# Kernel optimization log

Measured on AMD Instinct MI355X. Metric: run time of the kernel, lower is better.

The kernel has to match this reference:

```python
import jax, jax.numpy as jnp
import numpy as np

NUM_HEADS = 16
NEG_INF = -9e15


def setup_inputs() -> dict:
    key = jax.random.key(0)
    k1, k2, k3 = jax.random.split(key, 3)
    B, S, D = 2, 2048, 1024
    # xavier-uniform-ish init scale for weights
    lim_qkv = float(np.sqrt(6.0 / (D + 3 * D)))
    lim_o = float(np.sqrt(6.0 / (D + D)))
    return {
        "x": jax.random.normal(k1, (B, S, D), dtype=jnp.float32),
        "w_qkv": jax.random.uniform(k2, (3 * D, D), minval=-lim_qkv, maxval=lim_qkv, dtype=jnp.float32),
        "b_qkv": jnp.zeros((3 * D,), dtype=jnp.float32),
        "w_o": jax.random.uniform(k3, (D, D), minval=-lim_o, maxval=lim_o, dtype=jnp.float32),
        "b_o": jnp.zeros((D,), dtype=jnp.float32),
    }


def reference(x, w_qkv, b_qkv, w_o, b_o):
    B, S, D = x.shape
    H = NUM_HEADS
    hd = D // H
    # qkv projection: [B,S,3D]
    qkv = x @ w_qkv.T + b_qkv
    # -> [B, H, S, 3*hd], then split
    qkv = qkv.reshape(B, S, H, 3 * hd).transpose(0, 2, 1, 3)
    q, k, v = jnp.split(qkv, 3, axis=-1)  # each [B,H,S,hd]
    scale = 1.0 / jnp.sqrt(jnp.asarray(hd, dtype=x.dtype))
    logits = jnp.einsum("bhqd,bhkd->bhqk", q, k) * scale
    attn = jax.nn.softmax(logits, axis=-1)
    vals = jnp.einsum("bhqk,bhkd->bhqd", attn, v)
    vals = vals.transpose(0, 2, 1, 3).reshape(B, S, D)
    return vals @ w_o.T + b_o
```

## Files before the change

### kernel.cpp

```cpp
#include <hip/hip_runtime.h>
#include <math.h>

#define NHEADS 16
#define HD 64

typedef __attribute__((ext_vector_type(8))) _Float16 half8;
typedef __attribute__((ext_vector_type(4))) _Float16 half4;
typedef __attribute__((ext_vector_type(4))) float f32x4;
typedef __attribute__((ext_vector_type(16))) float f32x16;
typedef __attribute__((ext_vector_type(4))) unsigned int u32x4;

__device__ inline void load_lds16(const void* g, void* l) {
    __builtin_amdgcn_global_load_lds(
        (const __attribute__((address_space(1))) unsigned int*)g,
        (__attribute__((address_space(3))) unsigned int*)l, 16, 0, 0);
}
__device__ inline void pl32swap(unsigned int& x, unsigned int& y) {
    asm volatile("v_permlane32_swap_b32 %0, %1" : "+v"(x), "+v"(y));
}

#define NX  4194304
#define NWQ 3145728
#define NWO 1048576
__global__ void cvt_all(const float* __restrict__ x, const float* __restrict__ wq,
                        const float* __restrict__ wo, _Float16* __restrict__ xf,
                        _Float16* __restrict__ wqf, _Float16* __restrict__ wof) {
    int i = (blockIdx.x * blockDim.x + threadIdx.x) * 8;
    const float* src; _Float16* dst; int off;
    if (i < NX)            { src = x;  dst = xf;  off = i; }
    else if (i < NX + NWQ) { src = wq; dst = wqf; off = i - NX; }
    else                   { src = wo; dst = wof; off = i - (NX + NWQ); }
    float4 a = *(const float4*)(src + off);
    float4 b = *(const float4*)(src + off + 4);
    half8 h;
    h[0] = (_Float16)a.x; h[1] = (_Float16)a.y; h[2] = (_Float16)a.z; h[3] = (_Float16)a.w;
    h[4] = (_Float16)b.x; h[5] = (_Float16)b.y; h[6] = (_Float16)b.z; h[7] = (_Float16)b.w;
    *(half8*)(dst + off) = h;
}

#define GEMM_CORE(K)                                                                   \
    __shared__ __align__(1024) unsigned char smem[16384];                              \
    const int tid = threadIdx.x;                                                       \
    const int l = tid & 63, w = tid >> 6;                                              \
    const int wr = w >> 1, wc = w & 1;                                                 \
    const int nwg = gridDim.x * gridDim.y;                                             \
    const int bid = blockIdx.y * gridDim.x + blockIdx.x;                               \
    const int swz = (bid & 7) * (nwg >> 3) + (bid >> 3);                               \
    const int m0 = (swz / gridDim.x) * 128, n0 = (swz % gridDim.x) * 128;              \
    const int srow = tid >> 2;                                                         \
    const int schunk = (tid & 3) ^ ((srow >> 1) & 3);                                  \
    const size_t gA0 = (size_t)(m0 + srow) * K + schunk * 8;                           \
    const size_t gA1 = gA0 + (size_t)64 * K;                                           \
    const size_t gB0 = (size_t)(n0 + srow) * K + schunk * 8;                           \
    const size_t gB1 = gB0 + (size_t)64 * K;                                           \
    unsigned char* ldsW = smem + w * 1024;                                             \
    const int col16 = l & 15, kc = l >> 4;                                             \
    const int ra0 = wr * 64 + col16;                                                   \
    const int offA = ra0 * 64 + ((kc ^ ((ra0 >> 1) & 3)) * 16);                        \
    const int rb0 = wc * 64 + col16;                                                   \
    const int offB = rb0 * 64 + ((kc ^ ((rb0 >> 1) & 3)) * 16);                        \
    f32x4 acc[4][4] = {};                                                              \
    for (int k0 = 0; k0 < K; k0 += 32) {                                               \
        load_lds16(A + gA0 + k0, ldsW + 0);                                            \
        load_lds16(A + gA1 + k0, ldsW + 4096);                                         \
        load_lds16(B + gB0 + k0, ldsW + 8192);                                         \
        load_lds16(B + gB1 + k0, ldsW + 12288);                                       \
        __syncthreads();                                                               \
        half8 af[4], bf[4];                                                            \
        _Pragma("unroll")                                                              \
        for (int m = 0; m < 4; ++m) af[m] = *(const half8*)(smem + offA + m * 1024);   \
        _Pragma("unroll")                                                              \
        for (int n = 0; n < 4; ++n) bf[n] = *(const half8*)(smem + 8192 + offB + n * 1024); \
        _Pragma("unroll")                                                              \
        for (int m = 0; m < 4; ++m)                                                    \
            _Pragma("unroll")                                                          \
            for (int n = 0; n < 4; ++n)                                                \
                acc[m][n] = __builtin_amdgcn_mfma_f32_16x16x32_f16(af[m], bf[n], acc[m][n], 0, 0, 0); \
        __syncthreads();                                                               \
    }

__global__ __launch_bounds__(256, 2) void gemm_o(
    const _Float16* __restrict__ A, const _Float16* __restrict__ B,
    const float* __restrict__ bias, float* __restrict__ C,
    int M, int N, int K) {
    GEMM_CORE(K)
    const int rowb = m0 + wr * 64 + (l >> 4) * 4;
    const int colb = n0 + wc * 64 + col16;
    float bv[4];
    #pragma unroll
    for (int n = 0; n < 4; ++n) bv[n] = bias[colb + n * 16];
    #pragma unroll
    for (int m = 0; m < 4; ++m)
        #pragma unroll
        for (int j = 0; j < 4; ++j) {
            float* crow = C + (size_t)(rowb + m * 16 + j) * N + colb;
            #pragma unroll
            for (int n = 0; n < 4; ++n) crow[n * 16] = acc[m][n][j] + bv[n];
        }
}

#define QSCALE 0.18033688f
__global__ __launch_bounds__(256, 2) void gemm_qkv(
    const _Float16* __restrict__ A, const _Float16* __restrict__ B,
    const float* __restrict__ bias,
    _Float16* __restrict__ Qf, _Float16* __restrict__ Kf,
    _Float16* __restrict__ VfT, int K) {
    GEMM_CORE(K)
    const int rowb = m0 + wr * 64 + (l >> 4) * 4;
    const int colb = n0 + wc * 64 + col16;
    #pragma unroll
    for (int n = 0; n < 4; ++n) {
        int col = colb + n * 16;
        int h = col / 192;
        int rem = col - h * 192;
        int part = rem >> 6, d = rem & 63;
        float bv = bias[col];
        #pragma unroll
        for (int m = 0; m < 4; ++m) {
            int r0 = rowb + m * 16;
            int b = r0 >> 11, s0r = r0 & 2047;
            int bh = b * 16 + h;
            if (part == 0) {
                #pragma unroll
                for (int j = 0; j < 4; ++j)
                    Qf[((size_t)bh * 2048 + s0r + j) * 64 + d] =
                        (_Float16)((acc[m][n][j] + bv) * QSCALE);
            } else if (part == 1) {
                #pragma unroll
                for (int j = 0; j < 4; ++j)
                    Kf[((size_t)bh * 2048 + s0r + j) * 64 + d] = (_Float16)(acc[m][n][j] + bv);
            } else {
                half4 pk;
                pk[0] = (_Float16)(acc[m][n][0] + bv);
                pk[1] = (_Float16)(acc[m][n][1] + bv);
                pk[2] = (_Float16)(acc[m][n][2] + bv);
                pk[3] = (_Float16)(acc[m][n][3] + bv);
                *(half4*)&VfT[((size_t)bh * 64 + d) * 2048 + s0r] = pk;
            }
        }
    }
}

__global__ __launch_bounds__(256, 2) void mfma_attn(
    const _Float16* __restrict__ Qf, const _Float16* __restrict__ Kf,
    const _Float16* __restrict__ VfT, _Float16* __restrict__ vals) {
    __shared__ __align__(1024) unsigned char smem[32768];
    const int tid = threadIdx.x;
    const int l = tid & 63, w = tid >> 6;
    const int l31 = l & 31, hl = l >> 5;
    const int bh = blockIdx.y, q0 = blockIdx.x * 128;
    const int h = bh & 15, b = bh >> 4;

    half8 qf[4];
    {
        const _Float16* qp = Qf + ((size_t)bh * 2048 + q0 + w * 32 + l31) * 64 + hl * 8;
        #pragma unroll
        for (int c = 0; c < 4; ++c) qf[c] = *(const half8*)(qp + c * 16);
    }
    f32x16 zvec = {};
    f32x16 o0 = {}, o1 = {};
    float mshift = 0.f, lsum = 0.f;

    const _Float16* Kg = Kf + (size_t)bh * 2048 * 64;
    const _Float16* Vg = VfT + (size_t)bh * 64 * 2048;

    int offK[2], offV[2];
    #pragma unroll
    for (int i = 0; i < 2; ++i) {
        int row2 = w * 8 + i * 4 + (l >> 4);
        int slot = (l & 15) ^ (row2 & 15);
        int row = row2 * 2 + (slot >> 3);
        int chunk = slot & 7;
        offK[i] = row * 64 + chunk * 8;
        offV[i] = row * 2048 + chunk * 8;
    }
    const int sbase = (l31 & 1) * 8;
    const int xr = (l31 >> 1) & 15;
    const int rb0 = (l31 >> 1) * 256;

    #define STAGE(kt0, buf)                                                            \
        {                                                                              \
            unsigned char* bK = smem + (buf) * 8192 + w * 2048;                        \
            unsigned char* bV = smem + 16384 + (buf) * 8192 + w * 2048;                \
            load_lds16(Kg + (size_t)(kt0) * 64 + offK[0], bK);                         \
            load_lds16(Kg + (size_t)(kt0) * 64 + offK[1], bK + 1024);                  \
            load_lds16(Vg + (kt0) + offV[0], bV);                                      \
            load_lds16(Vg + (kt0) + offV[1], bV + 1024);                               \
        }

    STAGE(0, 0)
    __syncthreads();
    int cur = 0;
    for (int t = 0; t < 32; ++t) {
        if (t + 1 < 32) STAGE((t + 1) * 64, cur ^ 1)
        const unsigned char* Ksb = smem + cur * 8192;
        const unsigned char* Vsb = smem + 16384 + cur * 8192;

        f32x16 s0_, s1_;
        __builtin_amdgcn_s_setprio(1);
        {
            int chOff = ((sbase + hl) ^ xr) << 4;
            half8 k0 = *(const half8*)(Ksb + rb0 + chOff);
            half8 k1 = *(const half8*)(Ksb + rb0 + 4096 + chOff);
            s0_ = __builtin_amdgcn_mfma_f32_32x32x16_f16(k0, qf[0], zvec, 0, 0, 0);
            s1_ = __builtin_amdgcn_mfma_f32_32x32x16_f16(k1, qf[0], zvec, 0, 0, 0);
        }
        #pragma unroll
        for (int kc = 1; kc < 4; ++kc) {
            int chOff = ((sbase + kc * 2 + hl) ^ xr) << 4;
            half8 k0 = *(const half8*)(Ksb + rb0 + chOff);
            half8 k1 = *(const half8*)(Ksb + rb0 + 4096 + chOff);
            s0_ = __builtin_amdgcn_mfma_f32_32x32x16_f16(k0, qf[kc], s0_, 0, 0, 0);
            s1_ = __builtin_amdgcn_mfma_f32_32x32x16_f16(k1, qf[kc], s1_, 0, 0, 0);
        }
        __builtin_amdgcn_s_setprio(0);

        if (__any(mshift != 0.f)) {
            #pragma unroll
            for (int r = 0; r < 16; ++r) { s0_[r] -= mshift; s1_[r] -= mshift; }
        }

        float r0 = 0.f, r1 = 0.f, r2 = 0.f, r3 = 0.f;
        unsigned int a[2][8];
        #pragma unroll
        for (int j = 0; j < 8; ++j) {
            float p0 = __builtin_amdgcn_exp2f(s0_[2 * j]);
            float p1 = __builtin_amdgcn_exp2f(s0_[2 * j + 1]);
            float q0_ = __builtin_amdgcn_exp2f(s1_[2 * j]);
            float q1_ = __builtin_amdgcn_exp2f(s1_[2 * j + 1]);
            r0 += p0; r1 += p1; r2 += q0_; r3 += q1_;
            a[0][j] = __builtin_bit_cast(unsigned int, __builtin_amdgcn_cvt_pkrtz(p0, p1));
            a[1][j] = __builtin_bit_cast(unsigned int, __builtin_amdgcn_cvt_pkrtz(q0_, q1_));
        }
        float rsum = (r0 + r1) + (r2 + r3);

        if (__any(rsum > 32768.f)) {
            float pmax = s0_[0];
            #pragma unroll
            for (int r = 1; r < 16; ++r) pmax = fmaxf(pmax, s0_[r]);
            #pragma unroll
            for (int r = 0; r < 16; ++r) pmax = fmaxf(pmax, s1_[r]);
            pmax = fmaxf(pmax, __shfl_xor(pmax, 32, 64));
            float d_ = fmaxf(pmax, 0.f);
            float corr = __builtin_amdgcn_exp2f(-d_);
            #pragma unroll
            for (int r = 0; r < 16; ++r) { s0_[r] -= d_; s1_[r] -= d_; }
            #pragma unroll
            for (int r = 0; r < 16; ++r) { o0[r] *= corr; o1[r] *= corr; }
            lsum *= corr;
            mshift += d_;
            r0 = r1 = r2 = r3 = 0.f;
            #pragma unroll
            for (int j = 0; j < 8; ++j) {
                float p0 = __builtin_amdgcn_exp2f(s0_[2 * j]);
                float p1 = __builtin_amdgcn_exp2f(s0_[2 * j + 1]);
                float q0_ = __builtin_amdgcn_exp2f(s1_[2 * j]);
                float q1_ = __builtin_amdgcn_exp2f(s1_[2 * j + 1]);
                r0 += p0; r1 += p1; r2 += q0_; r3 += q1_;
                a[0][j] = __builtin_bit_cast(unsigned int, __builtin_amdgcn_cvt_pkrtz(p0, p1));
                a[1][j] = __builtin_bit_cast(unsigned int, __builtin_amdgcn_cvt_pkrtz(q0_, q1_));
            }
            rsum = (r0 + r1) + (r2 + r3);
        }
        lsum += rsum;

        #pragma unroll
        for (int c = 0; c < 2; ++c) {
            pl32swap(a[c][0], a[c][2]);
            pl32swap(a[c][1], a[c][3]);
            pl32swap(a[c][4], a[c][6]);
            pl32swap(a[c][5], a[c][7]);
        }

        __builtin_amdgcn_s_setprio(1);
        #pragma unroll
        for (int kk = 0; kk < 4; ++kk) {
            u32x4 pw;
            pw.x = a[kk >> 1][(kk & 1) * 4 + 0];
            pw.y = a[kk >> 1][(kk & 1) * 4 + 1];
            pw.z = a[kk >> 1][(kk & 1) * 4 + 2];
            pw.w = a[kk >> 1][(kk & 1) * 4 + 3];
            half8 pf = __builtin_bit_cast(half8, pw);
            int chOff = ((sbase + kk * 2 + hl) ^ xr) << 4;
            half8 v0 = *(const half8*)(Vsb + rb0 + chOff);
            half8 v1 = *(const half8*)(Vsb + rb0 + 4096 + chOff);
            o0 = __builtin_amdgcn_mfma_f32_32x32x16_f16(v0, pf, o0, 0, 0, 0);
            o1 = __builtin_amdgcn_mfma_f32_32x32x16_f16(v1, pf, o1, 0, 0, 0);
        }
        __builtin_amdgcn_s_setprio(0);
        __syncthreads();
        cur ^= 1;
    }

    lsum += __shfl_xor(lsum, 32, 64);
    float inv = 1.f / lsum;
    size_t orow = ((size_t)(b * 2048 + q0 + w * 32 + l31)) * 1024 + h * 64;
    #pragma unroll
    for (int dc = 0; dc < 2; ++dc) {
        const f32x16* op = dc ? &o1 : &o0;
        #pragma unroll
        for (int rq = 0; rq < 4; ++rq) {
            int d0 = dc * 32 + rq * 8 + hl * 4;
            half4 hv;
            #pragma unroll
            for (int j = 0; j < 4; ++j) hv[j] = (_Float16)((*op)[rq * 4 + j] * inv);
            *(half4*)(vals + orow + d0) = hv;
        }
    }
}

extern "C" void kernel_launch(void* const* d_in, const int* in_sizes, int n_in,
                              void* d_out, int out_size, void* d_ws, size_t ws_size,
                              hipStream_t stream) {
    const float* x     = (const float*)d_in[0];
    const float* w_qkv = (const float*)d_in[1];
    const float* b_qkv = (const float*)d_in[2];
    const float* w_o   = (const float*)d_in[3];
    const float* b_o   = (const float*)d_in[4];
    float* out = (float*)d_out;

    const int B = 2, S = 2048, D = 1024;
    const int M = B * S;
    const int N1 = 3 * D;
    const int BH = B * NHEADS;

    _Float16* xf  = (_Float16*)d_ws;
    _Float16* wqf = xf  + (size_t)M * D;
    _Float16* wof = wqf + (size_t)N1 * D;
    _Float16* Qf  = wof + (size_t)D * D;
    _Float16* Kf  = Qf  + (size_t)BH * S * HD;
    _Float16* VfT = Kf  + (size_t)BH * S * HD;
    _Float16* vals = xf;

    cvt_all<<<(NX + NWQ + NWO) / 2048, 256, 0, stream>>>(x, w_qkv, w_o, xf, wqf, wof);

    gemm_qkv<<<dim3(N1 / 128, M / 128), 256, 0, stream>>>(xf, wqf, b_qkv, Qf, Kf, VfT, D);

    mfma_attn<<<dim3(S / 128, BH), 256, 0, stream>>>(Qf, Kf, VfT, vals);

    gemm_o<<<dim3(D / 128, M / 128), 256, 0, stream>>>(vals, wof, b_o, out, M, D, D);
}
```

Baseline: 117.8 us.

## Split attention KV range across two wave groups and merge partial softmax

Doubles the attention block to 512 threads, so two groups of four waves each process alternating 64-key tiles for the same 128 queries. The LDS buffers double to 64KB to stage both groups' K/V tiles, and the loop count halves. At the end the second group writes its partial O, row sum and max to shared memory, and the first group rescales and merges them flash-decoding style before writing out. The aim is more waves in flight for latency hiding. The cost is a larger LDS footprint per block, which may limit occupancy, plus a merge step.

Result: slower. 126.8 us (+7.6%).

```diff
diff --git a/kernel.cpp b/kernel.cpp
--- a/kernel.cpp
+++ b/kernel.cpp
@@ -141,19 +141,20 @@
     }
 }
 
-__global__ __launch_bounds__(256, 2) void mfma_attn(
+__global__ __launch_bounds__(512, 4) void mfma_attn(
     const _Float16* __restrict__ Qf, const _Float16* __restrict__ Kf,
     const _Float16* __restrict__ VfT, _Float16* __restrict__ vals) {
-    __shared__ __align__(1024) unsigned char smem[32768];
+    __shared__ __align__(1024) unsigned char smem[65536];
     const int tid = threadIdx.x;
     const int l = tid & 63, w = tid >> 6;
+    const int wl = w & 3, hi = w >> 2;
     const int l31 = l & 31, hl = l >> 5;
     const int bh = blockIdx.y, q0 = blockIdx.x * 128;
     const int h = bh & 15, b = bh >> 4;
 
     half8 qf[4];
     {
-        const _Float16* qp = Qf + ((size_t)bh * 2048 + q0 + w * 32 + l31) * 64 + hl * 8;
+        const _Float16* qp = Qf + ((size_t)bh * 2048 + q0 + wl * 32 + l31) * 64 + hl * 8;
         #pragma unroll
         for (int c = 0; c < 4; ++c) qf[c] = *(const half8*)(qp + c * 16);
     }
@@ -167,7 +168,7 @@
     int offK[2], offV[2];
     #pragma unroll
     for (int i = 0; i < 2; ++i) {
-        int row2 = w * 8 + i * 4 + (l >> 4);
+        int row2 = wl * 8 + i * 4 + (l >> 4);
         int slot = (l & 15) ^ (row2 & 15);
         int row = row2 * 2 + (slot >> 3);
         int chunk = slot & 7;
@@ -178,23 +179,24 @@
     const int xr = (l31 >> 1) & 15;
     const int rb0 = (l31 >> 1) * 256;
 
-    #define STAGE(kt0, buf)                                                            \
+    #define STAGE(it, buf)                                                             \
         {                                                                              \
-            unsigned char* bK = smem + (buf) * 8192 + w * 2048;                        \
-            unsigned char* bV = smem + 16384 + (buf) * 8192 + w * 2048;                \
-            load_lds16(Kg + (size_t)(kt0) * 64 + offK[0], bK);                         \
-            load_lds16(Kg + (size_t)(kt0) * 64 + offK[1], bK + 1024);                  \
-            load_lds16(Vg + (kt0) + offV[0], bV);                                      \
-            load_lds16(Vg + (kt0) + offV[1], bV + 1024);                               \
+            int kb = ((it) * 2 + hi) * 64;                                             \
+            unsigned char* bK = smem + (buf) * 32768 + hi * 8192 + wl * 2048;          \
+            unsigned char* bV = bK + 16384;                                            \
+            load_lds16(Kg + (size_t)kb * 64 + offK[0], bK);                            \
+            load_lds16(Kg + (size_t)kb * 64 + offK[1], bK + 1024);                     \
+            load_lds16(Vg + kb + offV[0], bV);                                         \
+            load_lds16(Vg + kb + offV[1], bV + 1024);                                  \
         }
 
     STAGE(0, 0)
     __syncthreads();
     int cur = 0;
-    for (int t = 0; t < 32; ++t) {
-        if (t + 1 < 32) STAGE((t + 1) * 64, cur ^ 1)
-        const unsigned char* Ksb = smem + cur * 8192;
-        const unsigned char* Vsb = smem + 16384 + cur * 8192;
+    for (int t = 0; t < 16; ++t) {
+        if (t + 1 < 16) STAGE(t + 1, cur ^ 1)
+        const unsigned char* Ksb = smem + cur * 32768 + hi * 8192;
+        const unsigned char* Vsb = Ksb + 16384;
 
         f32x16 s0_, s1_;
         __builtin_amdgcn_s_setprio(1);
@@ -293,18 +295,41 @@
     }
 
     lsum += __shfl_xor(lsum, 32, 64);
-    float inv = 1.f / lsum;
-    size_t orow = ((size_t)(b * 2048 + q0 + w * 32 + l31)) * 1024 + h * 64;
-    #pragma unroll
-    for (int dc = 0; dc < 2; ++dc) {
-        const f32x16* op = dc ? &o1 : &o0;
-        #pragma unroll
-        for (int rq = 0; rq < 4; ++rq) {
-            int d0 = dc * 32 + rq * 8 + hl * 4;
-            half4 hv;
-            #pragma unroll
-            for (int j = 0; j < 4; ++j) hv[j] = (_Float16)((*op)[rq * 4 + j] * inv);
-            *(half4*)(vals + orow + d0) = hv;
+    float* mb = (float*)smem + wl * 2176;
+    if (hi == 1) {
+        #pragma unroll
+        for (int r = 0; r < 16; ++r) {
+            mb[r * 64 + l] = o0[r];
+            mb[(16 + r) * 64 + l] = o1[r];
+        }
+        mb[32 * 64 + l] = lsum;
+        mb[33 * 64 + l] = mshift;
+    }
+    __syncthreads();
+    if (hi == 0) {
+        float l1 = mb[32 * 64 + l], m1 = mb[33 * 64 + l];
+        float M = fmaxf(mshift, m1);
+        float f0 = __builtin_amdgcn_exp2f(mshift - M);
+        float f1 = __builtin_amdgcn_exp2f(m1 - M);
+        lsum = lsum * f0 + l1 * f1;
+        #pragma unroll
+        for (int r = 0; r < 16; ++r) {
+            o0[r] = o0[r] * f0 + mb[r * 64 + l] * f1;
+            o1[r] = o1[r] * f0 + mb[(16 + r) * 64 + l] * f1;
+        }
+        float inv = 1.f / lsum;
+        size_t orow = ((size_t)(b * 2048 + q0 + wl * 32 + l31)) * 1024 + h * 64;
+        #pragma unroll
+        for (int dc = 0; dc < 2; ++dc) {
+            const f32x16* op = dc ? &o1 : &o0;
+            #pragma unroll
+            for (int rq = 0; rq < 4; ++rq) {
+                int d0 = dc * 32 + rq * 8 + hl * 4;
+                half4 hv;
+                #pragma unroll
+                for (int j = 0; j < 4; ++j) hv[j] = (_Float16)((*op)[rq * 4 + j] * inv);
+                *(half4*)(vals + orow + d0) = hv;
+            }
         }
     }
 }
@@ -336,7 +361,7 @@
 
     gemm_qkv<<<dim3(N1 / 128, M / 128), 256, 0, stream>>>(xf, wqf, b_qkv, Qf, Kf, VfT, D);
 
-    mfma_attn<<<dim3(S / 128, BH), 256, 0, stream>>>(Qf, Kf, VfT, vals);
+    mfma_attn<<<dim3(S / 128, BH), 512, 0, stream>>>(Qf, Kf, VfT, vals);
 
     gemm_o<<<dim3(D / 128, M / 128), 256, 0, stream>>>(vals, wof, b_o, out, M, D, D);
 }
```
